# Kernel tuning notes

Measured on AMD Instinct MI355X. Metric: run time of the kernel, lower is better.

The kernel has to match this reference:

```python
import jax, jax.numpy as jnp
import numpy as np
from collections import deque

SIGMA_LOW = 0.02  # TreeFilter2D(sigma=0.02); high-level trees use sigma=1 (low_tree=False)


def bilinear_resize(x, oh, ow):
    # torch F.interpolate(mode='bilinear', align_corners=False)
    B, C, H, W = x.shape
    sy, sx = H / oh, W / ow
    ys = jnp.maximum((jnp.arange(oh, dtype=jnp.float32) + 0.5) * sy - 0.5, 0.0)
    xs = jnp.maximum((jnp.arange(ow, dtype=jnp.float32) + 0.5) * sx - 0.5, 0.0)
    y0 = jnp.clip(jnp.floor(ys).astype(jnp.int32), 0, H - 1)
    x0 = jnp.clip(jnp.floor(xs).astype(jnp.int32), 0, W - 1)
    y1 = jnp.minimum(y0 + 1, H - 1)
    x1 = jnp.minimum(x0 + 1, W - 1)
    wy = (ys - y0).reshape(oh, 1)
    wx = (xs - x0).reshape(1, ow)
    top, bot = x[:, :, y0, :], x[:, :, y1, :]
    v00, v01 = top[:, :, :, x0], top[:, :, :, x1]
    v10, v11 = bot[:, :, :, x0], bot[:, :, :, x1]
    return ((1 - wy) * (1 - wx)) * v00 + ((1 - wy) * wx) * v01 + (wy * (1 - wx)) * v10 + (wy * wx) * v11


def nearest_resize(x, oh, ow):
    B, C, H, W = x.shape
    yi = jnp.minimum((jnp.arange(oh) * (H / oh)).astype(jnp.int32), H - 1)
    xi = jnp.minimum((jnp.arange(ow) * (W / ow)).astype(jnp.int32), W - 1)
    return x[:, :, yi, :][:, :, :, xi]


def _mst_adj(feat, h, w):
    # Kruskal MST on 4-connected grid; edge weight = norm2_distance of features.
    n = h * w
    idx = np.arange(n).reshape(h, w)
    eu = np.concatenate([idx[:, :-1].ravel(), idx[:-1, :].ravel()])
    ev = np.concatenate([idx[:, 1:].ravel(), idx[1:, :].ravel()])
    f = feat.reshape(feat.shape[0], -1).astype(np.float64)
    d = ((f[:, eu] - f[:, ev]) ** 2).sum(axis=0)
    order = np.argsort(d, kind='stable')
    pa = np.arange(n)

    def find(a):
        r = a
        while pa[r] != r:
            r = pa[r]
        while pa[a] != r:
            pa[a], a = r, pa[a]
        return r

    adj = [[] for _ in range(n)]
    cnt = 0
    for e in order:
        u, v = int(eu[e]), int(ev[e])
        ru, rv = find(u), find(v)
        if ru != rv:
            pa[ru] = rv
            adj[u].append(v)
            adj[v].append(u)
            cnt += 1
            if cnt == n - 1:
                break
    return adj


def build_forest(embed):
    # embed: np [B,C,h,w] -> global parent array (ids b*n+i) + per-BFS-level node lists
    B, C, h, w = embed.shape
    n = h * w
    parent = np.arange(B * n)
    level = np.zeros(B * n, dtype=np.int64)
    for b in range(B):
        adj = _mst_adj(embed[b], h, w)
        lv = np.full(n, -1, dtype=np.int64)
        lv[0] = 0
        q = deque([0])
        while q:
            u = q.popleft()
            for v in adj[u]:
                if lv[v] < 0:
                    lv[v] = lv[u] + 1
                    parent[b * n + v] = b * n + u
                    q.append(v)
        level[b * n:(b + 1) * n] = lv
    d = int(level.max())
    levels = [np.nonzero(level == l)[0] for l in range(1, d + 1)]
    return jnp.asarray(parent), levels


def tree_filter(feature, embed, parent, levels, sigma):
    # feature [B,C,n], embed [B,Ce,n]; normalized tree filtering:
    # y_i = sum_j prod(path-edge-weights) x_j / sum_j prod(path-edge-weights)
    B, C, n = feature.shape
    ones = jnp.ones((B, 1, n), feature.dtype)
    xg = jnp.moveaxis(jnp.concatenate([feature, ones], axis=1), 0, 1).reshape(C + 1, B * n)
    eg = jnp.moveaxis(embed, 0, 1).reshape(embed.shape[1], B * n)
    wgt = jnp.exp(-((eg - eg[:, parent]) ** 2).sum(axis=0) / sigma)  # [B*n]; root entries unused
    # upward (leaf->root) subtree aggregation
    A = xg
    for idx in reversed(levels):
        A = A.at[:, parent[idx]].add(wgt[idx] * A[:, idx])
    # downward (root->leaf) completion
    F = A
    for idx in levels:
        F = F.at[:, idx].set(A[:, idx] + wgt[idx] * (F[:, parent[idx]] - wgt[idx] * A[:, idx]))
    y = F[:C] / F[C]
    return jnp.moveaxis(y.reshape(C, B, n), 0, 1)  # [B,C,n]


def setup_inputs() -> dict:
    key = jax.random.key(0)
    ks = jax.random.split(key, 6)
    B, K, h, w = 8, 4, 48, 48
    C = 512
    preds = jax.random.normal(ks[0], (B, K, h, w), jnp.float32)
    low_feats = jax.random.uniform(ks[1], (B, 3, 192, 192), jnp.float32) * 0.1
    hf1 = jax.random.normal(ks[2], (B, C, 24, 24), jnp.float32) * 0.05
    hf2 = jax.random.normal(ks[3], (B, C, 12, 12), jnp.float32) * 0.05
    hf3 = jax.random.normal(ks[4], (B, C, 6, 6), jnp.float32) * 0.05
    rois = (jax.random.uniform(ks[5], (B, 192, 192)) > 0.5).astype(jnp.float32)
    weight = jnp.asarray(0.4, jnp.float32)
    return {"preds": preds, "low_feats": low_feats, "high_feats_1": hf1,
            "high_feats_2": hf2, "high_feats_3": hf3, "unlabeled_ROIs": rois,
            "weight": weight}


def reference(preds, low_feats, high_feats_1, high_feats_2, high_feats_3, unlabeled_ROIs, weight):
    B, K, h, w = preds.shape
    low = bilinear_resize(low_feats, h, w)                     # no_grad in original
    roi = nearest_resize(unlabeled_ROIs[:, None], h, w)        # [B,1,h,w]
    N = roi.sum()
    prob = jax.nn.softmax(preds, axis=1)
    probf = prob.reshape(B, K, -1)
    roif = roi.reshape(B, 1, -1)

    parent0, lv0 = build_forest(np.asarray(low))
    AS = tree_filter(probf, low.reshape(B, low.shape[1], -1), parent0, lv0, SIGMA_LOW)

    loss = jnp.zeros((), preds.dtype)
    for hf in (high_feats_1, high_feats_2, high_feats_3):
        hfi = bilinear_resize(hf, h, w)
        p, lv = build_forest(np.asarray(hfi))
        AS_k = tree_filter(AS, hfi.reshape(B, hfi.shape[1], -1), p, lv, 1.0)
        loss = loss + (roif * jnp.abs(probf - AS_k)).sum()
    loss = jnp.where(N > 0, loss / N, loss)
    return weight * loss
```

## Files before the change

### kernel.cpp

```cpp
#include <hip/hip_runtime.h>
#include <math.h>


#define HH 48
#define WW 48
#define NN (HH*WW)
#define EHH (HH*(WW-1))
#define EEE (2*EHH)
#define BB 8
#define KK 4
#define TPB 256
#define TPE 512
#define TPW 1024
#define TPF 512
#define NPL 5
#define NPN 5
#define ESLOT (4*NN)
#define LVE (2*(NN-1))
#define RIPT ((LVE+TPW-1)/TPW)
#define SENTN 0xFFFFu
#define MAXT 12

#define SSTRIDE_W (4*NN+8)
#define PK_OFF 0
#define D_OFF (4*NN)

__device__ __forceinline__ void edge_uv(int e,int& u,int& v){
  if(e<EHH){ int r=e/(WW-1); int c=e-r*(WW-1); u=r*WW+c; v=u+1; }
  else     { int t=e-EHH; u=t; v=t+WW; }
}

__device__ __forceinline__ void pick_src(int f, const float* lowf, const float* hf1,
                                         const float* hf2, const float* hf3,
                                         const float*& src, int& sh, int& C){
  if(f==0){src=lowf; sh=192; C=3;}
  else if(f==1){src=hf1; sh=24; C=512;}
  else if(f==2){src=hf2; sh=12; C=512;}
  else        {src=hf3; sh=6;  C=512;}
}

__global__ __launch_bounds__(TPE) void k_edges(
  const float* __restrict__ lowf, const float* __restrict__ hf1,
  const float* __restrict__ hf2, const float* __restrict__ hf3,
  const float* __restrict__ preds, float* __restrict__ probf,
  double* __restrict__ pd_low, double* __restrict__ pd_hf, int nchunk)
{
  __shared__ float up[4*NN+64];
  __shared__ int   y0t[48], y1t[48];
  __shared__ float wyt[48];
  const int tid=threadIdx.x;
  const int nEB=8+24*nchunk;

  if(blockIdx.x>=nEB){
    int t=(blockIdx.x-nEB)*TPE+tid;
    if(t<BB*NN){
      int b=t/NN, i=t-b*NN;
      const float* p=preds+(size_t)b*KK*NN+i;
      float x0=p[0],x1=p[NN],x2=p[2*NN],x3=p[3*NN];
      float mx=fmaxf(fmaxf(x0,x1),fmaxf(x2,x3));
      float e0=expf(x0-mx),e1=expf(x1-mx),e2=expf(x2-mx),e3=expf(x3-mx);
      float s=((e0+e1)+(e2+e3));
      float* q=probf+(size_t)b*KK*NN+i;
      q[0]=e0/s; q[NN]=e1/s; q[2*NN]=e2/s; q[3*NN]=e3/s;
    }
    return;
  }

  int pidx, chunk, hfidx=0;
  if(blockIdx.x<8){ pidx=blockIdx.x; chunk=0; }
  else { int t=blockIdx.x-8; hfidx=t/nchunk; chunk=t-hfidx*nchunk; pidx=8+hfidx; }
  const int f=pidx>>3, b=pidx&7;
  const float* src; int sh,C;
  pick_src(f,lowf,hf1,hf2,hf3,src,sh,C);
  const int shw=sh*sh;
  const float* srcb=src+(size_t)b*C*shw;
  const int cpc=(f==0)?3:(512/nchunk);
  const int c_begin=chunk*cpc;
  const int c_end=(c_begin+cpc<C)?(c_begin+cpc):C;

  if(tid<48){
    float sy=(float)sh/48.0f;
    float ys=fmaxf(((float)tid+0.5f)*sy-0.5f,0.0f);
    int y0=(int)ys; if(y0>sh-1) y0=sh-1;
    int y1=y0+1; if(y1>sh-1) y1=sh-1;
    y0t[tid]=y0; y1t[tid]=y1; wyt[tid]=ys-(float)y0;
  }

  double accH[NPN], accV[NPN];
  #pragma unroll
  for(int j=0;j<NPN;j++){ accH[j]=0.0; accV[j]=0.0; }

  for(int c0=c_begin;c0<c_end;c0+=4){
    const int nc=(c_end-c0<4)?(c_end-c0):4;
    __syncthreads();
    for(int i=tid;i<NN;i+=TPE){
      int r=i/WW, c=i-r*WW;
      int y0=y0t[r], y1=y1t[r]; float wy=wyt[r];
      int x0=y0t[c], x1=y1t[c]; float wx=wyt[c];
      float w00=(1.0f-wy)*(1.0f-wx), w01=(1.0f-wy)*wx;
      float w10=wy*(1.0f-wx),        w11=wy*wx;
      int o00=y0*sh+x0, o01=y0*sh+x1, o10=y1*sh+x0, o11=y1*sh+x1;
      const float* pl=srcb+(size_t)c0*shw;
      for(int cc=0;cc<nc;cc++){
        const float* p=pl+(size_t)cc*shw;
        up[cc*NN+i]=w00*p[o00]+w01*p[o01]+w10*p[o10]+w11*p[o11];
      }
    }
    __syncthreads();
    #pragma unroll
    for(int j=0;j<NPN;j++){
      int u=tid+j*TPE;
      if(u<NN){
        int r=u/WW, c=u-r*WW;
        bool hOK=(c<WW-1), vOK=(r<HH-1);
        for(int cc=0;cc<nc;cc++){
          const float* pu=up+cc*NN+u;
          float a=pu[0], b1=pu[1], c1=pu[WW];
          if(hOK){ double d=(double)a-(double)b1; accH[j]=fma(d,d,accH[j]); }
          if(vOK){ double d=(double)a-(double)c1; accV[j]=fma(d,d,accV[j]); }
        }
      }
    }
  }
  double* outp=(f==0)? pd_low+(size_t)pidx*EEE
                     : pd_hf+((size_t)hfidx*nchunk+chunk)*EEE;
  #pragma unroll
  for(int j=0;j<NPN;j++){
    int u=tid+j*TPE;
    if(u<NN){
      int r=u/WW, c=u-r*WW;
      if(c<WW-1) outp[r*(WW-1)+c]=accH[j];
      if(r<HH-1) outp[EHH+u]=accV[j];
    }
  }
}

__global__ __launch_bounds__(TPB) void k_redux(
  const double* __restrict__ pd_low, const double* __restrict__ pd_hf,
  int nchunk, double* __restrict__ dkeyG)
{
  int t=blockIdx.x*TPB+threadIdx.x;
  if(t>=32*EEE) return;
  int pidx=t/EEE, e=t-pidx*EEE;
  double s;
  if(pidx<8) s=pd_low[(size_t)pidx*EEE+e];
  else {
    const double* p0=pd_hf+((size_t)(pidx-8)*nchunk)*EEE+e;
    s=0.0;
    for(int k=0;k<nchunk;k++) s+=p0[(size_t)k*EEE];
  }
  dkeyG[t]=s;
}

__global__ __launch_bounds__(TPW) void k_struct(
  const double* __restrict__ dkeyG, int* __restrict__ sbase,
  int* __restrict__ ancT, float* __restrict__ prodT)
{
  __shared__ __align__(16) char smem[123600];
  unsigned long long* keyE =(unsigned long long*)(smem+0);
  unsigned char*      mstf =(unsigned char*)(smem+36096);
  unsigned long long* best =(unsigned long long*)(smem+40608);
  int*                comp =(int*)(smem+59040);
  unsigned short*     uE   =(unsigned short*)(smem+68256);
  int*                lnk  =(int*)(smem+77472);
  float4*             adjw =(float4*)(smem+40608);
  unsigned char*      adjS =(unsigned char*)(smem+77472);
  int*                chunkS=(int*)(smem+79776);
  unsigned int*       eA   =(unsigned int*)(smem+0);
  unsigned int*       eB   =(unsigned int*)(smem+86688);
  int*                flags=(int*)(smem+123552);
  int*                ancA =(int*)(smem+0);
  float*              prmA =(float*)(smem+9216);
  int*                ancB =(int*)(smem+18432);
  float*              prmB =(float*)(smem+27648);

  const int tid=threadIdx.x;
  const int pidx=blockIdx.x;
  const int f=pidx>>3;
  const float sigma=(f==0)?0.02f:1.0f;
  const double* p0=dkeyG+(size_t)pidx*EEE;

  {
    for(int e=tid;e<EEE;e+=TPW){
      int u,v; edge_uv(e,u,v);
      uE[e]=(unsigned short)u;
      keyE[e]=(((unsigned long long)__double_as_longlong(p0[e]))&~0x1FFFull)
              |(unsigned long long)e;
      mstf[e]=0;
    }
    for(int i=tid;i<NN;i+=TPW){ comp[i]=i; best[i]=~0ull; lnk[i]=i; }
    if(tid==0) flags[1]=0;
    __syncthreads();

    for(int round=0;round<20;++round){
      for(int i=tid;i<NN;i+=TPW) lnk[i]=i;
      for(int e=tid;e<EEE;e+=TPW){
        int u=uE[e]; int v=(e<EHH)?u+1:u+WW;
        int cu=comp[u], cv=comp[v];
        if(cu!=cv){
          unsigned long long k=keyE[e];
          atomicMin(&best[cu],k);
          atomicMin(&best[cv],k);
        }
      }
      __syncthreads();
      for(int i=tid;i<NN;i+=TPW){
        if(comp[i]==i && best[i]!=~0ull){
          int e=(int)(best[i]&0x1FFFull);
          int u=uE[e]; int v=(e<EHH)?u+1:u+WW;
          int cu=comp[u], cv=comp[v];
          int other=(cu==i)?cv:cu;
          bool mutual=((best[other]&0x1FFFull)==(unsigned long long)e);
          if(!mutual || other<i){ lnk[i]=other; mstf[e]=1; flags[1]=1; }
        }
      }
      __syncthreads();
      if(flags[1]==0) break;
      {
        volatile int* vl=lnk;
        for(int i=tid;i<NN;i+=TPW){
          int x=comp[i];
          int p=vl[x];
          int gp=vl[p];
          while(p!=gp){
            vl[x]=gp;
            x=p; p=gp; gp=vl[p];
          }
          comp[i]=p;
        }
      }
      for(int i=tid;i<NN;i+=TPW) best[i]=~0ull;
      if(tid==0) flags[1]=0;
      __syncthreads();
    }
    __syncthreads();

    for(int i=tid;i<NN;i+=TPW){
      int r=i/WW, c=i-r*WW;
      int mask=0; float4 w; w.x=0.0f; w.y=0.0f; w.z=0.0f; w.w=0.0f;
      if(c>0    && mstf[r*(WW-1)+c-1]){ mask|=1; w.x=expf(-(float)p0[r*(WW-1)+c-1]/sigma); }
      if(c<WW-1 && mstf[r*(WW-1)+c])  { mask|=2; w.y=expf(-(float)p0[r*(WW-1)+c]/sigma); }
      if(r>0    && mstf[EHH+i-WW])    { mask|=4; w.z=expf(-(float)p0[EHH+i-WW]/sigma); }
      if(r<HH-1 && mstf[EHH+i])       { mask|=8; w.w=expf(-(float)p0[EHH+i]/sigma); }
      adjw[i]=w;
      adjS[i]=(unsigned char)mask;
    }
    if(tid==0) flags[2]=0;
    __syncthreads();
  }

  {
    const int m0=adjS[0];
    const int d0=(m0&1)?0:((m0&2)?1:((m0&4)?2:3));
    const int e0=d0;

    for(int t=tid;t<ESLOT;t+=TPW){
      int u=t>>2, d=t&3;
      unsigned int pk=0;
      if(adjS[u]&(1<<d)){
        int v=(d==0)?u-1:(d==1)?u+1:(d==2)?u-WW:u+WW;
        int rd=d^1;
        int mv=adjS[v];
        int nd=rd;
        #pragma unroll
        for(int k2=4;k2>=1;k2--){ int dd=(rd+k2)&3; if(mv&(1<<dd)) nd=dd; }
        int ne=(v<<2)|nd;
        unsigned int nxt=(ne==e0)?SENTN:(unsigned int)ne;
        pk=(nxt<<16)|1u;
      }
      eA[t]=pk;
    }
    __syncthreads();

    unsigned int* P=eA; unsigned int* Q=eB;
    for(int r2=0;r2<13;r2++){
      for(int t=tid;t<ESLOT;t+=TPW){
        unsigned int pk=P[t];
        unsigned int dist=pk&0xFFFFu, nxt=pk>>16;
        if(dist && nxt!=SENTN){
          unsigned int pk2=P[nxt];
          dist+=pk2&0xFFFFu;
          nxt=pk2>>16;
          pk=(nxt<<16)|dist;
        }
        Q[t]=pk;
      }
      __syncthreads();
      unsigned int* tmp=P; P=Q; Q=tmp;
    }
    for(int t=tid;t<ESLOT;t+=TPW){
      unsigned int dist=P[t]&0xFFFFu;
      Q[t]=dist?(unsigned int)(LVE-(int)dist):0xFFFFFFFFu;
    }
    __syncthreads();

    int* scanA=(int*)P;
    for(int t=tid;t<ESLOT;t+=TPW){
      unsigned int pos=Q[t];
      if(pos!=0xFFFFFFFFu){
        int u=t>>2, d=t&3;
        int v=(d==0)?u-1:(d==1)?u+1:(d==2)?u-WW:u+WW;
        unsigned int rpos=Q[(v<<2)|(d^1)];
        scanA[pos]=(pos<rpos)?1:-1;
      }
    }
    __syncthreads();

    const int base=tid*RIPT;
    int vals[RIPT]; int lsum=0;
    #pragma unroll
    for(int j=0;j<RIPT;j++){
      int p=base+j;
      int v=(p<LVE)?scanA[p]:0;
      lsum+=v; vals[j]=lsum;
    }
    const int lane=tid&63, wid=tid>>6;
    int x=lsum;
    #pragma unroll
    for(int off=1;off<64;off<<=1){
      int y=__shfl_up(x,off,64);
      if(lane>=off) x+=y;
    }
    if(lane==63) chunkS[wid]=x;
    __syncthreads();
    if(wid==0 && lane<16){
      int w=chunkS[lane];
      #pragma unroll
      for(int off=1;off<16;off<<=1){
        int y=__shfl_up(w,off,64);
        if(lane>=off) w+=y;
      }
      chunkS[lane]=w;
    }
    __syncthreads();
    const int waveoff=(wid>0)?chunkS[wid-1]:0;
    const int myoff=x+waveoff-lsum;
    int mymax=0;
    #pragma unroll
    for(int j=0;j<RIPT;j++){
      int p=base+j;
      if(p<LVE){ int s=vals[j]+myoff; scanA[p]=s; if(s>mymax) mymax=s; }
    }
    if(mymax>0) atomicMax(&flags[2],mymax);
    __syncthreads();

    int* sp=sbase+(size_t)pidx*SSTRIDE_W;
    int4* g_pk=(int4*)(sp+PK_OFF);
    if(tid==0){
      g_pk[0]=make_int4(0,__float_as_int(0.0f),0,0);
      sp[D_OFF]=flags[2];
    }
    for(int t=tid;t<ESLOT;t+=TPW){
      unsigned int pos=Q[t];
      if(pos!=0xFFFFFFFFu){
        int u=t>>2, d=t&3;
        int v=(d==0)?u-1:(d==1)?u+1:(d==2)?u-WW:u+WW;
        unsigned int rpos=Q[(v<<2)|(d^1)];
        if(pos<rpos){
          float4 w4=adjw[u];
          float w=(d==0)?w4.x:(d==1)?w4.y:(d==2)?w4.z:w4.w;
          g_pk[v]=make_int4(u,__float_as_int(w),scanA[pos],0);
        }
      }
    }
    __syncthreads();
  }

  {
    const int* sp=sbase+(size_t)pidx*SSTRIDE_W;
    const int4* g_pk=(const int4*)(sp+PK_OFF);
    const int maxD=flags[2];
    int T=1; while((1<<T)<=maxD) T++;
    int* gA=ancT+(size_t)pidx*MAXT*NN;
    float* gP=prodT+(size_t)pidx*MAXT*NN;
    int* aP=ancA; int* aQ=ancB; float* pP=prmA; float* pQ=prmB;
    for(int i=tid;i<NN;i+=TPW){
      int4 rec=g_pk[i];
      aP[i]=rec.x; pP[i]=__int_as_float(rec.y);
      gA[i]=rec.x; gP[i]=pP[i];
    }
    __syncthreads();
    for(int t=1;t<T;t++){
      for(int i=tid;i<NN;i+=TPW){
        int a=aP[i];
        int a2=aP[a]; float pr=pP[i]*pP[a];
        aQ[i]=a2; pQ[i]=pr;
        gA[(size_t)t*NN+i]=a2; gP[(size_t)t*NN+i]=pr;
      }
      __syncthreads();
      { int* t1=aP; aP=aQ; aQ=t1; float* t2=pP; pP=pQ; pQ=t2; }
    }
  }
}

__global__ __launch_bounds__(TPF) void k_fchan(
  const float* __restrict__ X, float* __restrict__ Fout,
  const int* __restrict__ sbase, const int* __restrict__ ancT,
  const float* __restrict__ prodT, int pidx0, int dv)
{
  __shared__ float S[NN];
  __shared__ float Sb[NN];
  const int tid=threadIdx.x;
  const int pg=blockIdx.x/5, c=blockIdx.x%5;
  const int pidx=pidx0+pg;
  const int xb=pg&7;
  const int* sp=sbase+(size_t)pidx*SSTRIDE_W;
  const int4* g_pk=(const int4*)(sp+PK_OFF);
  const int maxD=sp[D_OFF];
  int T=1; while((1<<T)<=maxD) T++;
  const int* ancP=ancT+(size_t)pidx*MAXT*NN;
  const float* prmP=prodT+(size_t)pidx*MAXT*NN;

  int dep[NPL]; float wv[NPL];
  #pragma unroll
  for(int j=0;j<NPL;j++){
    int i=tid+j*TPF;
    if(i<NN){
      int4 rec=g_pk[i];
      dep[j]=rec.z; wv[j]=__int_as_float(rec.y);
      float val=1.0f;
      if(c<4){
        if(dv){
          float inv=1.0f/X[((size_t)xb*5+4)*NN+i];
          val=X[((size_t)xb*5+c)*NN+i]*inv;
        } else {
          val=X[((size_t)xb*KK+c)*NN+i];
        }
      }
      S[i]=val;
    } else { dep[j]=-1; wv[j]=0.0f; }
  }
  __syncthreads();

  for(int t=0;t<T;t++){
    float sn[NPL]; int aj[NPL]; float pj[NPL];
    #pragma unroll
    for(int j=0;j<NPL;j++){
      int i=tid+j*TPF;
      if(i<NN){ sn[j]=S[i]; aj[j]=ancP[(size_t)t*NN+i]; pj[j]=prmP[(size_t)t*NN+i]; }
      else { sn[j]=0.0f; aj[j]=0; pj[j]=0.0f; }
    }
    __syncthreads();
    int bit=1<<t;
    #pragma unroll
    for(int j=0;j<NPL;j++){
      if(dep[j]>=bit) atomicAdd(&S[aj[j]], pj[j]*sn[j]);
    }
    __syncthreads();
  }

  #pragma unroll
  for(int j=0;j<NPL;j++){
    int i=tid+j*TPF;
    if(i<NN){ float fq=1.0f-wv[j]*wv[j]; Sb[i]=fq*S[i]; }
  }
  __syncthreads();

  float* Sp=Sb; float* Sq=S;
  for(int t=0;t<T;t++){
    float bn[NPL];
    #pragma unroll
    for(int j=0;j<NPL;j++){
      int i=tid+j*TPF;
      if(i<NN){
        int a=ancP[(size_t)t*NN+i]; float ai=prmP[(size_t)t*NN+i];
        bn[j]=fmaf(ai,Sp[a],Sp[i]);
      } else bn[j]=0.0f;
    }
    __syncthreads();
    #pragma unroll
    for(int j=0;j<NPL;j++){
      int i=tid+j*TPF;
      if(i<NN) Sq[i]=bn[j];
    }
    __syncthreads();
    { float* tmp=Sp; Sp=Sq; Sq=tmp; }
  }
  float* o=Fout+(size_t)blockIdx.x*NN;
  for(int i=tid;i<NN;i+=TPF) o[i]=Sp[i];
}

__global__ __launch_bounds__(TPB) void k_loss(
  const float* __restrict__ FB, const float* __restrict__ probf,
  const float* __restrict__ rois, float* __restrict__ partials)
{
  __shared__ float red[TPB];
  const int tid=threadIdx.x;
  const int fb=blockIdx.x;
  const int b=fb&7;
  const float* pb=probf+(size_t)b*KK*NN;
  float part=0.0f;
  for(int i=tid;i<NN;i+=TPB){
    int r=i/WW, c2=i-r*WW;
    float roi=rois[(size_t)b*(192*192)+(4*r)*192+(4*c2)];
    float inv=1.0f/FB[((size_t)fb*5+4)*NN+i];
    float s=fabsf(pb[i]      -FB[((size_t)fb*5+0)*NN+i]*inv)
          + fabsf(pb[NN+i]   -FB[((size_t)fb*5+1)*NN+i]*inv)
          + fabsf(pb[2*NN+i] -FB[((size_t)fb*5+2)*NN+i]*inv)
          + fabsf(pb[3*NN+i] -FB[((size_t)fb*5+3)*NN+i]*inv);
    part+=roi*s;
  }
  red[tid]=part; __syncthreads();
  for(int s2=TPB/2;s2>0;s2>>=1){ if(tid<s2) red[tid]+=red[tid+s2]; __syncthreads(); }
  if(tid==0) partials[fb]=red[0];
}

__global__ __launch_bounds__(TPB) void k_final(const float* __restrict__ rois,
    const float* __restrict__ partials, const float* __restrict__ wt,
    float* __restrict__ out)
{
  __shared__ float red[TPB];
  const int tid=threadIdx.x;
  float n=0.0f;
  for(int t=tid;t<BB*NN;t+=TPB){
    int b=t/NN, i=t-b*NN; int r=i/WW, c=i-r*WW;
    n += rois[(size_t)b*(192*192)+(4*r)*192+(4*c)];
  }
  red[tid]=n; __syncthreads();
  for(int s=TPB/2;s>0;s>>=1){ if(tid<s) red[tid]+=red[tid+s]; __syncthreads(); }
  if(tid==0){
    float loss=0.0f;
    for(int j=0;j<3*BB;j++) loss+=partials[j];
    float N=red[0];
    out[0]=wt[0]*((N>0.0f)?(loss/N):loss);
  }
}

extern "C" void kernel_launch(void* const* d_in, const int* in_sizes, int n_in,
                              void* d_out, int out_size, void* d_ws, size_t ws_size,
                              hipStream_t stream) {
  (void)in_sizes; (void)n_in; (void)out_size;
  const float* preds=(const float*)d_in[0];
  const float* lowf =(const float*)d_in[1];
  const float* hf1  =(const float*)d_in[2];
  const float* hf2  =(const float*)d_in[3];
  const float* hf3  =(const float*)d_in[4];
  const float* rois =(const float*)d_in[5];
  const float* wt   =(const float*)d_in[6];
  float* out=(float*)d_out;

  char* ws=(char*)d_ws;
  float* partials=(float*)ws;
  float* probf=(float*)(ws+256);
  size_t sb_off=256+(size_t)2*BB*KK*NN*4;
  int*   sbase=(int*)(ws+sb_off);
  size_t dk_off=sb_off+(size_t)32*SSTRIDE_W*4;
  double* dkeyG=(double*)(ws+dk_off);
  size_t pl_off=dk_off+(size_t)32*EEE*8;
  double* pd_low=(double*)(ws+pl_off);
  size_t ph_off=pl_off+(size_t)8*EEE*8;
  double* pd_hf=(double*)(ws+ph_off);

  int*   ancT =(int*)  (ws+ph_off);
  float* prodT=(float*)(ws+ph_off+(size_t)32*MAXT*NN*4);
  float* FA   =(float*)(ws+ph_off+(size_t)2*32*MAXT*NN*4);
  float* FB   =(float*)(ws+ph_off+(size_t)2*32*MAXT*NN*4+(size_t)40*NN*4);

  int nchunk=32;
  if(ph_off+(size_t)24*32*EEE*8>ws_size) nchunk=16;

  const int nEB=8+24*nchunk;
  const int nSM=(BB*NN+TPE-1)/TPE;
  k_edges<<<nEB+nSM,TPE,0,stream>>>(lowf,hf1,hf2,hf3,preds,probf,pd_low,pd_hf,nchunk);
  k_redux<<<(32*EEE+TPB-1)/TPB,TPB,0,stream>>>(pd_low,pd_hf,nchunk,dkeyG);
  k_struct<<<32,TPW,0,stream>>>(dkeyG,sbase,ancT,prodT);
  k_fchan<<<40,TPF,0,stream>>>(probf,FA,sbase,ancT,prodT,0,0);
  k_fchan<<<120,TPF,0,stream>>>(FA,FB,sbase,ancT,prodT,8,1);
  k_loss<<<3*BB,TPB,0,stream>>>(FB,probf,rois,partials);
  k_final<<<1,TPB,0,stream>>>(rois,partials,wt,out);
}
```

Before: 212.2 us.

## Compact Euler-tour edge slots, pack ancestor tables, fuse final reduction

After: 206.0 us, median of 2. 2.9% less time.

```diff
diff --git a/kernel.cpp b/kernel.cpp
--- a/kernel.cpp
+++ b/kernel.cpp
@@ -15,9 +15,9 @@
 #define TPF 512
 #define NPL 5
 #define NPN 5
-#define ESLOT (4*NN)
 #define LVE (2*(NN-1))
 #define RIPT ((LVE+TPW-1)/TPW)
+#define NIPT ((NN+TPW-1)/TPW)
 #define SENTN 0xFFFFu
 #define MAXT 12
 
@@ -137,9 +137,10 @@
 
 __global__ __launch_bounds__(TPB) void k_redux(
   const double* __restrict__ pd_low, const double* __restrict__ pd_hf,
-  int nchunk, double* __restrict__ dkeyG)
+  int nchunk, double* __restrict__ dkeyG, int* __restrict__ cnt)
 {
   int t=blockIdx.x*TPB+threadIdx.x;
+  if(t==0) *cnt=0;
   if(t>=32*EEE) return;
   int pidx=t/EEE, e=t-pidx*EEE;
   double s;
@@ -154,20 +155,22 @@
 
 __global__ __launch_bounds__(TPW) void k_struct(
   const double* __restrict__ dkeyG, int* __restrict__ sbase,
-  int* __restrict__ ancT, float* __restrict__ prodT)
+  int2* __restrict__ apT)
 {
   __shared__ __align__(16) char smem[123600];
   unsigned long long* keyE =(unsigned long long*)(smem+0);
   unsigned char*      mstf =(unsigned char*)(smem+36096);
   unsigned long long* best =(unsigned long long*)(smem+40608);
   int*                comp =(int*)(smem+59040);
-  unsigned short*     uE   =(unsigned short*)(smem+68256);
+  unsigned short*     uEdg =(unsigned short*)(smem+68256);
   int*                lnk  =(int*)(smem+77472);
   float4*             adjw =(float4*)(smem+40608);
   unsigned char*      adjS =(unsigned char*)(smem+77472);
   int*                chunkS=(int*)(smem+79776);
   unsigned int*       eA   =(unsigned int*)(smem+0);
-  unsigned int*       eB   =(unsigned int*)(smem+86688);
+  unsigned int*       eB   =(unsigned int*)(smem+18432);
+  unsigned short*     uDE  =(unsigned short*)(smem+83872);
+  int*                nodeoff=(int*)(smem+93088);
   int*                flags=(int*)(smem+123552);
   int*                ancA =(int*)(smem+0);
   float*              prmA =(float*)(smem+9216);
@@ -179,11 +182,12 @@
   const int f=pidx>>3;
   const float sigma=(f==0)?0.02f:1.0f;
   const double* p0=dkeyG+(size_t)pidx*EEE;
+  const int lane=tid&63, wid=tid>>6;
 
   {
     for(int e=tid;e<EEE;e+=TPW){
       int u,v; edge_uv(e,u,v);
-      uE[e]=(unsigned short)u;
+      uEdg[e]=(unsigned short)u;
       keyE[e]=(((unsigned long long)__double_as_longlong(p0[e]))&~0x1FFFull)
               |(unsigned long long)e;
       mstf[e]=0;
@@ -195,7 +199,7 @@
     for(int round=0;round<20;++round){
       for(int i=tid;i<NN;i+=TPW) lnk[i]=i;
       for(int e=tid;e<EEE;e+=TPW){
-        int u=uE[e]; int v=(e<EHH)?u+1:u+WW;
+        int u=uEdg[e]; int v=(e<EHH)?u+1:u+WW;
         int cu=comp[u], cv=comp[v];
         if(cu!=cv){
           unsigned long long k=keyE[e];
@@ -207,7 +211,7 @@
       for(int i=tid;i<NN;i+=TPW){
         if(comp[i]==i && best[i]!=~0ull){
           int e=(int)(best[i]&0x1FFFull);
-          int u=uE[e]; int v=(e<EHH)?u+1:u+WW;
+          int u=uEdg[e]; int v=(e<EHH)?u+1:u+WW;
           int cu=comp[u], cv=comp[v];
           int other=(cu==i)?cv:cu;
           bool mutual=((best[other]&0x1FFFull)==(unsigned long long)e);
@@ -250,34 +254,70 @@
   }
 
   {
-    const int m0=adjS[0];
-    const int d0=(m0&1)?0:((m0&2)?1:((m0&4)?2:3));
-    const int e0=d0;
-
-    for(int t=tid;t<ESLOT;t+=TPW){
-      int u=t>>2, d=t&3;
-      unsigned int pk=0;
-      if(adjS[u]&(1<<d)){
+    {
+      const int base=tid*NIPT;
+      int dg[NIPT], incl[NIPT]; int lsum=0;
+      #pragma unroll
+      for(int j=0;j<NIPT;j++){
+        int i=base+j;
+        dg[j]=(i<NN)?__popc((int)adjS[i]):0;
+        lsum+=dg[j]; incl[j]=lsum;
+      }
+      int x=lsum;
+      #pragma unroll
+      for(int off=1;off<64;off<<=1){
+        int y=__shfl_up(x,off,64);
+        if(lane>=off) x+=y;
+      }
+      if(lane==63) chunkS[wid]=x;
+      __syncthreads();
+      if(wid==0 && lane<16){
+        int w=chunkS[lane];
+        #pragma unroll
+        for(int off=1;off<16;off<<=1){
+          int y=__shfl_up(w,off,64);
+          if(lane>=off) w+=y;
+        }
+        chunkS[lane]=w;
+      }
+      __syncthreads();
+      const int waveoff=(wid>0)?chunkS[wid-1]:0;
+      const int myoff=x+waveoff-lsum;
+      #pragma unroll
+      for(int j=0;j<NIPT;j++){
+        int i=base+j;
+        if(i<NN) nodeoff[i]=myoff+incl[j]-dg[j];
+      }
+    }
+    __syncthreads();
+
+    for(int u=tid;u<NN;u+=TPW){
+      int mu=adjS[u];
+      int off=nodeoff[u];
+      int m=mu;
+      while(m){
+        int d=__ffs(m)-1; m&=m-1;
+        int ce=off+__popc(mu&((1<<d)-1));
         int v=(d==0)?u-1:(d==1)?u+1:(d==2)?u-WW:u+WW;
         int rd=d^1;
         int mv=adjS[v];
         int nd=rd;
         #pragma unroll
         for(int k2=4;k2>=1;k2--){ int dd=(rd+k2)&3; if(mv&(1<<dd)) nd=dd; }
-        int ne=(v<<2)|nd;
-        unsigned int nxt=(ne==e0)?SENTN:(unsigned int)ne;
-        pk=(nxt<<16)|1u;
-      }
-      eA[t]=pk;
+        int ne=nodeoff[v]+__popc(mv&((1<<nd)-1));
+        unsigned int nxt=(ne==0)?SENTN:(unsigned int)ne;
+        uDE[ce]=(unsigned short)((u<<2)|d);
+        eA[ce]=(nxt<<16)|1u;
+      }
     }
     __syncthreads();
 
     unsigned int* P=eA; unsigned int* Q=eB;
     for(int r2=0;r2<13;r2++){
-      for(int t=tid;t<ESLOT;t+=TPW){
+      for(int t=tid;t<LVE;t+=TPW){
         unsigned int pk=P[t];
         unsigned int dist=pk&0xFFFFu, nxt=pk>>16;
-        if(dist && nxt!=SENTN){
+        if(nxt!=SENTN){
           unsigned int pk2=P[nxt];
           dist+=pk2&0xFFFFu;
           nxt=pk2>>16;
@@ -288,21 +328,20 @@
       __syncthreads();
       unsigned int* tmp=P; P=Q; Q=tmp;
     }
-    for(int t=tid;t<ESLOT;t+=TPW){
+    for(int t=tid;t<LVE;t+=TPW){
       unsigned int dist=P[t]&0xFFFFu;
-      Q[t]=dist?(unsigned int)(LVE-(int)dist):0xFFFFFFFFu;
+      Q[t]=(unsigned int)(LVE-(int)dist);
     }
     __syncthreads();
 
     int* scanA=(int*)P;
-    for(int t=tid;t<ESLOT;t+=TPW){
+    for(int t=tid;t<LVE;t+=TPW){
       unsigned int pos=Q[t];
-      if(pos!=0xFFFFFFFFu){
-        int u=t>>2, d=t&3;
-        int v=(d==0)?u-1:(d==1)?u+1:(d==2)?u-WW:u+WW;
-        unsigned int rpos=Q[(v<<2)|(d^1)];
-        scanA[pos]=(pos<rpos)?1:-1;
-      }
+      int ud=uDE[t]; int u=ud>>2, d=ud&3;
+      int v=(d==0)?u-1:(d==1)?u+1:(d==2)?u-WW:u+WW;
+      int rce=nodeoff[v]+__popc(adjS[v]&((1<<(d^1))-1));
+      unsigned int rpos=Q[rce];
+      scanA[pos]=(pos<rpos)?1:-1;
     }
     __syncthreads();
 
@@ -314,7 +353,6 @@
       int v=(p<LVE)?scanA[p]:0;
       lsum+=v; vals[j]=lsum;
     }
-    const int lane=tid&63, wid=tid>>6;
     int x=lsum;
     #pragma unroll
     for(int off=1;off<64;off<<=1){
@@ -350,17 +388,16 @@
       g_pk[0]=make_int4(0,__float_as_int(0.0f),0,0);
       sp[D_OFF]=flags[2];
     }
-    for(int t=tid;t<ESLOT;t+=TPW){
+    for(int t=tid;t<LVE;t+=TPW){
       unsigned int pos=Q[t];
-      if(pos!=0xFFFFFFFFu){
-        int u=t>>2, d=t&3;
-        int v=(d==0)?u-1:(d==1)?u+1:(d==2)?u-WW:u+WW;
-        unsigned int rpos=Q[(v<<2)|(d^1)];
-        if(pos<rpos){
-          float4 w4=adjw[u];
-          float w=(d==0)?w4.x:(d==1)?w4.y:(d==2)?w4.z:w4.w;
-          g_pk[v]=make_int4(u,__float_as_int(w),scanA[pos],0);
-        }
+      int ud=uDE[t]; int u=ud>>2, d=ud&3;
+      int v=(d==0)?u-1:(d==1)?u+1:(d==2)?u-WW:u+WW;
+      int rce=nodeoff[v]+__popc(adjS[v]&((1<<(d^1))-1));
+      unsigned int rpos=Q[rce];
+      if(pos<rpos){
+        float4 w4=adjw[u];
+        float w=(d==0)?w4.x:(d==1)?w4.y:(d==2)?w4.z:w4.w;
+        g_pk[v]=make_int4(u,__float_as_int(w),scanA[pos],0);
       }
     }
     __syncthreads();
@@ -371,13 +408,12 @@
     const int4* g_pk=(const int4*)(sp+PK_OFF);
     const int maxD=flags[2];
     int T=1; while((1<<T)<=maxD) T++;
-    int* gA=ancT+(size_t)pidx*MAXT*NN;
-    float* gP=prodT+(size_t)pidx*MAXT*NN;
+    int2* gAP=apT+(size_t)pidx*MAXT*NN;
     int* aP=ancA; int* aQ=ancB; float* pP=prmA; float* pQ=prmB;
     for(int i=tid;i<NN;i+=TPW){
       int4 rec=g_pk[i];
       aP[i]=rec.x; pP[i]=__int_as_float(rec.y);
-      gA[i]=rec.x; gP[i]=pP[i];
+      gAP[i]=make_int2(rec.x,rec.y);
     }
     __syncthreads();
     for(int t=1;t<T;t++){
@@ -385,7 +421,7 @@
         int a=aP[i];
         int a2=aP[a]; float pr=pP[i]*pP[a];
         aQ[i]=a2; pQ[i]=pr;
-        gA[(size_t)t*NN+i]=a2; gP[(size_t)t*NN+i]=pr;
+        gAP[(size_t)t*NN+i]=make_int2(a2,__float_as_int(pr));
       }
       __syncthreads();
       { int* t1=aP; aP=aQ; aQ=t1; float* t2=pP; pP=pQ; pQ=t2; }
@@ -395,8 +431,8 @@
 
 __global__ __launch_bounds__(TPF) void k_fchan(
   const float* __restrict__ X, float* __restrict__ Fout,
-  const int* __restrict__ sbase, const int* __restrict__ ancT,
-  const float* __restrict__ prodT, int pidx0, int dv)
+  const int* __restrict__ sbase, const int2* __restrict__ apT,
+  int pidx0, int dv)
 {
   __shared__ float S[NN];
   __shared__ float Sb[NN];
@@ -408,8 +444,7 @@
   const int4* g_pk=(const int4*)(sp+PK_OFF);
   const int maxD=sp[D_OFF];
   int T=1; while((1<<T)<=maxD) T++;
-  const int* ancP=ancT+(size_t)pidx*MAXT*NN;
-  const float* prmP=prodT+(size_t)pidx*MAXT*NN;
+  const int2* apP=apT+(size_t)pidx*MAXT*NN;
 
   int dep[NPL]; float wv[NPL];
   #pragma unroll
@@ -437,7 +472,10 @@
     #pragma unroll
     for(int j=0;j<NPL;j++){
       int i=tid+j*TPF;
-      if(i<NN){ sn[j]=S[i]; aj[j]=ancP[(size_t)t*NN+i]; pj[j]=prmP[(size_t)t*NN+i]; }
+      if(i<NN){
+        int2 ap=apP[(size_t)t*NN+i];
+        sn[j]=S[i]; aj[j]=ap.x; pj[j]=__int_as_float(ap.y);
+      }
       else { sn[j]=0.0f; aj[j]=0; pj[j]=0.0f; }
     }
     __syncthreads();
@@ -463,8 +501,8 @@
     for(int j=0;j<NPL;j++){
       int i=tid+j*TPF;
       if(i<NN){
-        int a=ancP[(size_t)t*NN+i]; float ai=prmP[(size_t)t*NN+i];
-        bn[j]=fmaf(ai,Sp[a],Sp[i]);
+        int2 ap=apP[(size_t)t*NN+i];
+        bn[j]=fmaf(__int_as_float(ap.y),Sp[ap.x],Sp[i]);
       } else bn[j]=0.0f;
     }
     __syncthreads();
@@ -482,9 +520,11 @@
 
 __global__ __launch_bounds__(TPB) void k_loss(
   const float* __restrict__ FB, const float* __restrict__ probf,
-  const float* __restrict__ rois, float* __restrict__ partials)
+  const float* __restrict__ rois, float* __restrict__ partials,
+  const float* __restrict__ wt, float* __restrict__ out, int* __restrict__ cnt)
 {
   __shared__ float red[TPB];
+  __shared__ int lastS;
   const int tid=threadIdx.x;
   const int fb=blockIdx.x;
   const int b=fb&7;
@@ -502,19 +542,19 @@
   }
   red[tid]=part; __syncthreads();
   for(int s2=TPB/2;s2>0;s2>>=1){ if(tid<s2) red[tid]+=red[tid+s2]; __syncthreads(); }
-  if(tid==0) partials[fb]=red[0];
-}
-
-__global__ __launch_bounds__(TPB) void k_final(const float* __restrict__ rois,
-    const float* __restrict__ partials, const float* __restrict__ wt,
-    float* __restrict__ out)
-{
-  __shared__ float red[TPB];
-  const int tid=threadIdx.x;
+  if(tid==0){
+    partials[fb]=red[0];
+    __threadfence();
+    int old=atomicAdd(cnt,1);
+    lastS=(old==3*BB-1);
+  }
+  __syncthreads();
+  if(!lastS) return;
+
   float n=0.0f;
   for(int t=tid;t<BB*NN;t+=TPB){
-    int b=t/NN, i=t-b*NN; int r=i/WW, c=i-r*WW;
-    n += rois[(size_t)b*(192*192)+(4*r)*192+(4*c)];
+    int b2=t/NN, i=t-b2*NN; int r=i/WW, c=i-r*WW;
+    n += rois[(size_t)b2*(192*192)+(4*r)*192+(4*c)];
   }
   red[tid]=n; __syncthreads();
   for(int s=TPB/2;s>0;s>>=1){ if(tid<s) red[tid]+=red[tid+s]; __syncthreads(); }
@@ -541,6 +581,7 @@
 
   char* ws=(char*)d_ws;
   float* partials=(float*)ws;
+  int*   cnt=(int*)(ws+128);
   float* probf=(float*)(ws+256);
   size_t sb_off=256+(size_t)2*BB*KK*NN*4;
   int*   sbase=(int*)(ws+sb_off);
@@ -551,10 +592,9 @@
   size_t ph_off=pl_off+(size_t)8*EEE*8;
   double* pd_hf=(double*)(ws+ph_off);
 
-  int*   ancT =(int*)  (ws+ph_off);
-  float* prodT=(float*)(ws+ph_off+(size_t)32*MAXT*NN*4);
-  float* FA   =(float*)(ws+ph_off+(size_t)2*32*MAXT*NN*4);
-  float* FB   =(float*)(ws+ph_off+(size_t)2*32*MAXT*NN*4+(size_t)40*NN*4);
+  int2*  apT=(int2*)(ws+ph_off);
+  float* FA =(float*)(ws+ph_off+(size_t)32*MAXT*NN*8);
+  float* FB =(float*)(ws+ph_off+(size_t)32*MAXT*NN*8+(size_t)40*NN*4);
 
   int nchunk=32;
   if(ph_off+(size_t)24*32*EEE*8>ws_size) nchunk=16;
@@ -562,10 +602,9 @@
   const int nEB=8+24*nchunk;
   const int nSM=(BB*NN+TPE-1)/TPE;
   k_edges<<<nEB+nSM,TPE,0,stream>>>(lowf,hf1,hf2,hf3,preds,probf,pd_low,pd_hf,nchunk);
-  k_redux<<<(32*EEE+TPB-1)/TPB,TPB,0,stream>>>(pd_low,pd_hf,nchunk,dkeyG);
-  k_struct<<<32,TPW,0,stream>>>(dkeyG,sbase,ancT,prodT);
-  k_fchan<<<40,TPF,0,stream>>>(probf,FA,sbase,ancT,prodT,0,0);
-  k_fchan<<<120,TPF,0,stream>>>(FA,FB,sbase,ancT,prodT,8,1);
-  k_loss<<<3*BB,TPB,0,stream>>>(FB,probf,rois,partials);
-  k_final<<<1,TPB,0,stream>>>(rois,partials,wt,out);
-}
+  k_redux<<<(32*EEE+TPB-1)/TPB,TPB,0,stream>>>(pd_low,pd_hf,nchunk,dkeyG,cnt);
+  k_struct<<<32,TPW,0,stream>>>(dkeyG,sbase,apT);
+  k_fchan<<<40,TPF,0,stream>>>(probf,FA,sbase,apT,0,0);
+  k_fchan<<<120,TPF,0,stream>>>(FA,FB,sbase,apT,8,1);
+  k_loss<<<3*BB,TPB,0,stream>>>(FB,probf,rois,partials,wt,out,cnt);
+}
```
